# Optimization experiments

Measured on AMD Instinct MI355X. Metric: run time of the kernel, lower is better.

The kernel has to match this reference:

```python
import jax, jax.numpy as jnp
import numpy as np

PAD, BOS = 0, 1
EPS = 1e-08


def _lstm_cell(xt, h, c, wih, whh, bih, bhh):
    z = xt @ wih.T + h @ whh.T + bih + bhh
    i, f, g, o = jnp.split(z, 4, axis=-1)  # torch gate order i,f,g,o
    c = jax.nn.sigmoid(f) * c + jax.nn.sigmoid(i) * jnp.tanh(g)
    h = jax.nn.sigmoid(o) * jnp.tanh(c)
    return h, c


def _run_lstm(emb, wih, whh, bih, bhh):
    B, H = emb.shape[0], whh.shape[1]
    def step(carry, xt):
        h, c = _lstm_cell(xt, carry[0], carry[1], wih, whh, bih, bhh)
        return (h, c), h
    init = (jnp.zeros((B, H), emb.dtype), jnp.zeros((B, H), emb.dtype))
    (hT, cT), outs = jax.lax.scan(step, init, jnp.swapaxes(emb, 0, 1))
    return jnp.swapaxes(outs, 0, 1), hT, cT


def setup_inputs() -> dict:
    key = jax.random.key(0)
    V, H, B, S, T = 32000, 256, 8, 200, 51
    ks = jax.random.split(key, 24)
    def n(i, shape, s=0.02):
        return jax.random.normal(ks[i], shape, jnp.float32) * s
    x = jax.random.randint(ks[0], (B, S), 1, V)
    x = x.at[:, -1].set(V - 1)  # pins extended vocab size to 2V
    labels = jax.random.randint(ks[1], (B, T), 1, V)
    return {
        "x": x, "labels": labels, "ext_vocab_size": 2 * V,
        "emb_enc": n(2, (V, H)).at[PAD].set(0.0),
        "wih_f": n(3, (4 * H, H)), "whh_f": n(4, (4 * H, H)),
        "bih_f": jnp.zeros((4 * H,), jnp.float32), "bhh_f": jnp.zeros((4 * H,), jnp.float32),
        "wih_b": n(5, (4 * H, H)), "whh_b": n(6, (4 * H, H)),
        "bih_b": jnp.zeros((4 * H,), jnp.float32), "bhh_b": jnp.zeros((4 * H,), jnp.float32),
        "w_sel1": n(7, (H, 2 * H)), "b_sel1": jnp.zeros((H,), jnp.float32),
        "w_sel2": n(8, (1, H)), "b_sel2": jnp.zeros((1,), jnp.float32),
        "w_rh": n(9, (H, 2 * H)), "b_rh": jnp.zeros((H,), jnp.float32),
        "w_rc": n(10, (H, 2 * H)), "b_rc": jnp.zeros((H,), jnp.float32),
        "emb_dec": n(11, (V, H)).at[PAD].set(0.0),
        "wih_d": n(12, (4 * H, 3 * H)), "whh_d": n(13, (4 * H, H)),
        "bih_d": jnp.zeros((4 * H,), jnp.float32), "bhh_d": jnp.zeros((4 * H,), jnp.float32),
        "w_attn": n(14, (H, 4 * H)), "b_attn": jnp.zeros((H,), jnp.float32),
        "w_attn_v": n(15, (1, H)),
        "w_ptr": n(16, (1, 3 * H)), "b_ptr": jnp.zeros((1,), jnp.float32),
        "w_gen": n(17, (V, H)), "b_gen": jnp.zeros((V,), jnp.float32),
        "w_cov": n(18, (H, 1)), "b_cov": jnp.zeros((H,), jnp.float32),
    }


def reference(x, labels, ext_vocab_size, emb_enc, wih_f, whh_f, bih_f, bhh_f,
              wih_b, whh_b, bih_b, bhh_b, w_sel1, b_sel1, w_sel2, b_sel2,
              w_rh, b_rh, w_rc, b_rc, emb_dec, wih_d, whh_d, bih_d, bhh_d,
              w_attn, b_attn, w_attn_v, w_ptr, b_ptr, w_gen, b_gen, w_cov, b_cov):
    B, S = x.shape
    V, H = w_gen.shape
    # ---- Encoder: BiLSTM (no padding -> packing is identity; eval -> no dropout)
    emb = emb_enc[x]  # [B,S,H]
    out_f, h_f, c_f = _run_lstm(emb, wih_f, whh_f, bih_f, bhh_f)
    out_b_r, h_b, c_b = _run_lstm(emb[:, ::-1], wih_b, whh_b, bih_b, bhh_b)
    enc_out = jnp.concatenate([out_f, out_b_r[:, ::-1]], axis=-1)  # [B,S,2H]
    copy_probs = jax.nn.sigmoid(
        (jnp.tanh(enc_out @ w_sel1.T + b_sel1) @ w_sel2.T + b_sel2)[..., 0])  # [B,S]
    # ---- bidirectional state reduction
    h0 = jax.nn.relu(jnp.concatenate([h_f, h_b], -1) @ w_rh.T + b_rh)
    c0 = jax.nn.relu(jnp.concatenate([c_f, c_b], -1) @ w_rc.T + b_rc)
    # ---- Decoder loop (teacher forcing): inputs = [BOS, labels[:,1:T-1]]
    dec_in = jnp.concatenate(
        [jnp.full((B, 1), BOS, labels.dtype), labels[:, 1:-1]], axis=1)  # [B,T-1]
    mask_cp = (copy_probs > EPS).astype(jnp.float32)
    rows = jnp.arange(B)[:, None]

    def step(carry, tok):
        h, c, cov = carry
        cov_feat = cov[..., None] * w_cov[:, 0] + b_cov  # [B,S,H]
        feats = jnp.concatenate(
            [enc_out, jnp.broadcast_to(h[:, None, :], (B, S, H)), cov_feat], axis=-1)
        e = jnp.tanh(feats @ w_attn.T + b_attn)           # [B,S,H]
        attn = jax.nn.softmax(e @ w_attn_v[0], axis=1)    # [B,S]
        attn = attn * mask_cp
        attn = attn / (attn.sum(1, keepdims=True) + 1e-10)
        cov = cov + attn
        ctx = jnp.einsum('bs,bsd->bd', attn, enc_out)     # [B,2H]
        h, c = _lstm_cell(jnp.concatenate([emb_dec[tok], ctx], -1), h, c,
                          wih_d, whh_d, bih_d, bhh_d)
        p_gen = jax.nn.sigmoid(jnp.concatenate([ctx, h], -1) @ w_ptr.T + b_ptr)  # [B,1]
        vocab_dist = jax.nn.softmax(h @ w_gen.T + b_gen, axis=-1)  # [B,V]
        dist = jnp.zeros((B, ext_vocab_size), jnp.float32)
        dist = dist.at[:, :V].set(p_gen * vocab_dist)
        dist = dist.at[rows, x].add((1.0 - p_gen) * attn)  # pointer/copy scatter-add
        return (h, c, cov), dist

    cov0 = jnp.zeros((B, S), jnp.float32)
    _, outs = jax.lax.scan(step, (h0, c0, cov0), dec_in.T)
    outputs = jnp.swapaxes(outs, 0, 1)  # [B,T-1,EV]
    # ---- loss (faithful: CE treats the mixture distribution as logits)
    targets = labels[:, 1:]
    logp = jax.nn.log_softmax(outputs, axis=-1)
    nll = -jnp.take_along_axis(logp, targets[..., None], axis=-1)[..., 0]
    valid = (targets != PAD).astype(jnp.float32)
    loss_ce = (nll * valid).sum() / valid.sum()
    m = (x != PAD).astype(jnp.float32)
    lp = jnp.clip(jnp.log(copy_probs), -100.0, None)
    l1p = jnp.clip(jnp.log1p(-copy_probs), -100.0, None)
    bce = -(m * lp + (1.0 - m) * l1p)
    loss = loss_ce + 1.0 * (bce * m).sum() / m.sum()
    return outputs, loss
```

## Files before the change

### kernel.cpp

```cpp
#include <hip/hip_runtime.h>
#include <hip/hip_bf16.h>
#include <stdint.h>


#define DEVI __device__ __forceinline__
#define AT_RLX __ATOMIC_RELAXED
#define SC_AGT __HIP_MEMORY_SCOPE_AGENT

static constexpr size_t OFF_ACC   = 0;
static constexpr size_t OFF_FLAGE = 4;
static constexpr size_t OFF_FLAGD = 36;
static constexpr size_t ZERO_FLOATS = 200;
static constexpr size_t OFF_CTX   = 256;
static constexpr size_t OFF_EMB   = 4352;
static constexpr size_t OFF_HSEL  = OFF_EMB;
static constexpr size_t OFF_PREF  = OFF_EMB  + 409600;
static constexpr size_t OFF_PREB  = OFF_PREF + 1638400;
static constexpr size_t OFF_BIAS  = OFF_PREB + 1638400;
static constexpr size_t OFF_HB    = OFF_BIAS + 3072;
static constexpr size_t OFF_HFIN  = OFF_HB   + 8192;
static constexpr size_t OFF_CFIN  = OFF_HFIN + 4096;
static constexpr size_t OFF_ENCOUT= OFF_CFIN + 4096;
static constexpr size_t OFF_MASK  = OFF_ENCOUT + 819200;
static constexpr size_t OFF_C0    = OFF_MASK + 1600;
static constexpr size_t OFF_EP    = OFF_C0   + 2048;
static constexpr size_t OFF_WCP   = OFF_EP   + 409600;
static constexpr size_t OFF_BCP   = OFF_WCP  + 256;
static constexpr size_t OFF_DEMB  = OFF_BCP  + 256;
static constexpr size_t OFF_DPRE  = OFF_DEMB + 102400;
static constexpr size_t OFF_HBUF  = OFF_DPRE + 409600;
static constexpr size_t OFF_CS    = OFF_HBUF + 4096;
static constexpr size_t OFF_HS    = OFF_CS   + 204800;
static constexpr size_t OFF_AS    = OFF_HS   + 102400;
static constexpr size_t OFF_PG    = OFF_AS   + 80000;
static constexpr size_t OFF_PE    = OFF_PG   + 512;

DEVI float sigf(float x)      { return 1.0f / (1.0f + __expf(-x)); }
DEVI float tanh_fast(float x) { return 1.0f - 2.0f / (1.0f + __expf(2.0f * x)); }
DEVI float pick4(float z, float x1, float x2, float x3, int mm) {
  return mm == 0 ? z : (mm == 1 ? x1 : (mm == 2 ? x2 : x3));
}
DEVI float ald(const float* p)  { return __hip_atomic_load((float*)p, AT_RLX, SC_AGT); }
DEVI void  ast(float* p, float v){ __hip_atomic_store(p, v, AT_RLX, SC_AGT); }

DEVI void fbar(int* flags, int g, int n, int val) {
  __syncthreads();
  if ((int)threadIdx.x == 0)
    __hip_atomic_store(flags + g, val, AT_RLX, SC_AGT);
  if ((int)threadIdx.x < n && (int)threadIdx.x != g) {
    while (__hip_atomic_load(flags + threadIdx.x, AT_RLX, SC_AGT) < val)
      __builtin_amdgcn_s_sleep(1);
  }
  __syncthreads();
}

__global__ __launch_bounds__(256) void k_biassum(
    const float* bih_f, const float* bhh_f, const float* bih_b, const float* bhh_b,
    const float* bih_d, const float* bhh_d, float* ws) {
  int i = blockIdx.x * 256 + threadIdx.x;
  int which = i >> 10, jj = i & 1023;
  float v = (which == 0) ? bih_f[jj] + bhh_f[jj]
          : (which == 1) ? bih_b[jj] + bhh_b[jj]
                         : bih_d[jj] + bhh_d[jj];
  ws[OFF_BIAS + i] = v;
}

__global__ __launch_bounds__(256) void k_embed(
    const int* xin, const int* labels, const float* emb_enc, const float* emb_dec, float* ws) {
  int r = blockIdx.x, h = threadIdx.x;
  if (r < 1600) {
    int t = r >> 3, b = r & 7;
    ws[OFF_EMB + (size_t)r * 256 + h] = emb_enc[(size_t)xin[b * 200 + t] * 256 + h];
  } else {
    int r2 = r - 1600;
    int t = r2 >> 3, b = r2 & 7;
    int tok = (t == 0) ? 1 : labels[b * 51 + t];
    ws[OFF_DEMB + (size_t)r2 * 256 + h] = emb_dec[(size_t)tok * 256 + h];
  }
}

template<int BM, int BN, int TM, int TN, int CMAP, int ACT, int AMAP>
__global__ __launch_bounds__(256) void k_gemm(
    const float* __restrict__ A, const float* __restrict__ B,
    const float* __restrict__ bias, float* __restrict__ C,
    int M, int K, int ldb, int ldc) {
  __shared__ float As[16][BM];
  __shared__ float Bs[16][BN];
  const int tid = threadIdx.x;
  const int tx = tid & 15, ty = tid >> 4;
  const int m0 = blockIdx.x * BM, n0 = blockIdx.y * BN;
  float acc[TM][TN];
#pragma unroll
  for (int i = 0; i < TM; ++i)
#pragma unroll
    for (int q = 0; q < TN; ++q) acc[i][q] = 0.f;

  for (int kk = 0; kk < K; kk += 16) {
#pragma unroll
    for (int e = tid; e < BM * 4; e += 256) {
      int m = e >> 2, k4 = (e & 3) * 4;
      int gm0 = m0 + m;
      float4 v = {0.f, 0.f, 0.f, 0.f};
      if (gm0 < M) {
        int gm = AMAP ? (((199 - (gm0 >> 3)) << 3) + (gm0 & 7)) : gm0;
        v = *(const float4*)(A + (size_t)gm * K + kk + k4);
      }
      As[k4 + 0][m] = v.x; As[k4 + 1][m] = v.y; As[k4 + 2][m] = v.z; As[k4 + 3][m] = v.w;
    }
#pragma unroll
    for (int e = tid; e < BN * 4; e += 256) {
      int n = e >> 2, k4 = (e & 3) * 4;
      float4 v = *(const float4*)(B + (size_t)(n0 + n) * ldb + kk + k4);
      Bs[k4 + 0][n] = v.x; Bs[k4 + 1][n] = v.y; Bs[k4 + 2][n] = v.z; Bs[k4 + 3][n] = v.w;
    }
    __syncthreads();
#pragma unroll
    for (int k = 0; k < 16; ++k) {
      float a[TM], bv[TN];
#pragma unroll
      for (int i = 0; i < TM; ++i) a[i] = As[k][ty * TM + i];
#pragma unroll
      for (int q = 0; q < TN; ++q) bv[q] = Bs[k][tx * TN + q];
#pragma unroll
      for (int i = 0; i < TM; ++i)
#pragma unroll
        for (int q = 0; q < TN; ++q) acc[i][q] += a[i] * bv[q];
    }
    __syncthreads();
  }
#pragma unroll
  for (int i = 0; i < TM; ++i) {
    int gm = m0 + ty * TM + i;
    if (gm >= M) continue;
    size_t base;
    if (CMAP == 1) { int t = gm >> 3, b = gm & 7; base = (size_t)(b * 50 + t) * 64000; }
    else            base = (size_t)gm * ldc;
#pragma unroll
    for (int q = 0; q < TN; ++q) {
      int n = n0 + tx * TN + q;
      float v = acc[i][q] + bias[n];
      if (ACT == 1) v = tanh_fast(v);
      C[base + n] = v;
    }
  }
}

__global__ __launch_bounds__(512, 1) void k_encoder(
    const float* __restrict__ whh_f, const float* __restrict__ whh_b, float* __restrict__ ws) {
  __shared__ float hs[8 * 288];
  __shared__ float zs[512];
  const int dir = blockIdx.x >> 4;
  const int p   = blockIdx.x & 15;
  const int u0  = p * 16;
  const float* whh = dir ? whh_b : whh_f;
  const float* pre = ws + (dir ? OFF_PREB : OFF_PREF);
  int* flags = (int*)(ws + OFF_FLAGE) + dir * 16;
  const int tid = threadIdx.x;
  const int r = tid >> 3, kc = tid & 7;
  const int gt = r >> 4, ui = r & 15;
  const int j = gt * 256 + u0 + ui;
  float4 W[8];
  {
    const float* wr = whh + (size_t)j * 256 + kc * 32;
#pragma unroll
    for (int q = 0; q < 8; ++q) W[q] = *(const float4*)(wr + q * 4);
  }
  const int ui2 = tid & 15, b2 = tid >> 4;
  float c_reg = 0.f;
  float* hBa = ws + OFF_HB;
  float* enc = ws + OFF_ENCOUT;

  for (int t = 0; t < 200; ++t) {
    float pre_v = pre[((size_t)t * 8 + kc) * 1024 + j];
    float acc[8];
#pragma unroll
    for (int b = 0; b < 8; ++b) acc[b] = 0.f;
    if (t > 0) {
      {
        float* src = hBa + (size_t)((((t + 1) & 1) * 2 + dir) * 2048) + tid * 4;
        float v0 = ald(src + 0);
        float v1 = ald(src + 1);
        float v2 = ald(src + 2);
        float v3 = ald(src + 3);
        int kk0 = (tid * 4) & 255, bb = tid >> 6;
        float* dst = &hs[bb * 288 + (kk0 >> 5) * 36 + (kk0 & 31)];
        dst[0] = v0; dst[1] = v1; dst[2] = v2; dst[3] = v3;
      }
      __syncthreads();
      const float* hrow = &hs[kc * 36];
#pragma unroll
      for (int b = 0; b < 8; ++b) {
        const float* hbp = hrow + b * 288;
#pragma unroll
        for (int q = 0; q < 8; ++q) {
          float4 h4 = *(const float4*)(hbp + q * 4);
          acc[b] = fmaf(W[q].x, h4.x, acc[b]);
          acc[b] = fmaf(W[q].y, h4.y, acc[b]);
          acc[b] = fmaf(W[q].z, h4.z, acc[b]);
          acc[b] = fmaf(W[q].w, h4.w, acc[b]);
        }
      }
    }
    {
      bool h4b = (kc & 4) != 0;
#pragma unroll
      for (int i = 0; i < 4; ++i) {
        float send = h4b ? acc[i] : acc[i + 4];
        float keep = h4b ? acc[i + 4] : acc[i];
        acc[i] = keep + __shfl_xor(send, 4);
      }
      bool h2b = (kc & 2) != 0;
#pragma unroll
      for (int i = 0; i < 2; ++i) {
        float send = h2b ? acc[i] : acc[i + 2];
        float keep = h2b ? acc[i + 2] : acc[i];
        acc[i] = keep + __shfl_xor(send, 2);
      }
      bool h1b = (kc & 1) != 0;
      {
        float send = h1b ? acc[0] : acc[1];
        float keep = h1b ? acc[1] : acc[0];
        acc[0] = keep + __shfl_xor(send, 1);
      }
    }
    zs[tid] = acc[0] + pre_v;
    __syncthreads();
    if (tid < 128) {
      int i0 = ui2 * 8 + b2;
      float zi = zs[i0], zf = zs[128 + i0], zg = zs[256 + i0], zo = zs[384 + i0];
      float cn = sigf(zf) * c_reg + sigf(zi) * tanh_fast(zg);
      float hn = sigf(zo) * tanh_fast(cn);
      c_reg = cn;
      int uu = u0 + ui2;
      ast(hBa + (size_t)(((t & 1) * 2 + dir) * 2048) + b2 * 256 + uu, hn);
      int s = dir ? (199 - t) : t;
      enc[((size_t)b2 * 200 + s) * 512 + dir * 256 + uu] = hn;
      if (t == 199) {
        ws[OFF_HFIN + (size_t)(dir * 8 + b2) * 256 + uu] = hn;
        ws[OFF_CFIN + (size_t)(dir * 8 + b2) * 256 + uu] = cn;
      }
    }
    if (t < 199) fbar(flags, p, 16, t + 1);
  }
}

__global__ __launch_bounds__(64) void k_selbce(
    const float* w_sel2, const float* b_sel2, const int* xin, float* ws) {
  int r = blockIdx.x, lane = threadIdx.x;
  float pacc = 0.f;
#pragma unroll
  for (int i = 0; i < 4; ++i) {
    int k = lane + 64 * i;
    pacc += ws[OFF_HSEL + (size_t)r * 256 + k] * w_sel2[k];
  }
#pragma unroll
  for (int m = 1; m < 64; m <<= 1) pacc += __shfl_xor(pacc, m);
  if (lane == 0) {
    float cp = sigf(pacc + b_sel2[0]);
    ws[OFF_MASK + r] = (cp > 1e-8f) ? 1.f : 0.f;
    int b = r / 200, s = r % 200;
    float m = (xin[b * 200 + s] != 0) ? 1.f : 0.f;
    if (m > 0.f) {
      float lp = fmaxf(logf(cp), -100.f);
      atomicAdd(ws + OFF_ACC + 2, -lp);
    }
    atomicAdd(ws + OFF_ACC + 3, m);
  }
}

__global__ __launch_bounds__(256) void k_wcp(
    const float* w_attn, const float* w_cov, const float* b_cov, float* ws) {
  int jj = threadIdx.x;
  float a = 0.f, c = 0.f;
  for (int h = 0; h < 256; ++h) {
    float w = w_attn[(size_t)jj * 1024 + 768 + h];
    a += w * w_cov[h];
    c += w * b_cov[h];
  }
  ws[OFF_WCP + jj] = a;
  ws[OFF_BCP + jj] = c;
}

__global__ __launch_bounds__(256) void k_h0c0(
    const float* w_rh, const float* b_rh, const float* w_rc, const float* b_rc, float* ws) {
  int b = blockIdx.x, jj = threadIdx.x;
  const float* hf  = ws + OFF_HFIN + (size_t)b * 256;
  const float* hbk = ws + OFF_HFIN + 2048 + (size_t)b * 256;
  const float* cf  = ws + OFF_CFIN + (size_t)b * 256;
  const float* cbk = ws + OFF_CFIN + 2048 + (size_t)b * 256;
  float ah = b_rh[jj], ac = b_rc[jj];
  for (int k = 0; k < 256; ++k) {
    ah += hf[k] * w_rh[(size_t)jj * 512 + k];
    ac += cf[k] * w_rc[(size_t)jj * 512 + k];
  }
  for (int k = 0; k < 256; ++k) {
    ah += hbk[k] * w_rh[(size_t)jj * 512 + 256 + k];
    ac += cbk[k] * w_rc[(size_t)jj * 512 + 256 + k];
  }
  ws[OFF_C0 + (size_t)b * 256 + jj] = fmaxf(ac, 0.f);
  ws[OFF_HBUF + (size_t)b * 256 + jj] = fmaxf(ah, 0.f);
}

__global__ __launch_bounds__(512, 1) void k_decoder(
    const float* __restrict__ wih_d, const float* __restrict__ whh_d,
    const float* __restrict__ w_attn, const float* __restrict__ w_attn_v,
    float* __restrict__ ws) {
  __shared__ float hc_s[8 * 768];
  __shared__ float h_pad[264];
  __shared__ float hw_q[64];
  __shared__ float e_s[256];
  __shared__ float at_s[256], cv_s[256], msk_s[256];
  __shared__ float zs_l[256];
  __shared__ float wcq_s[64], bcq_s[64], wvq_s[64];
  __shared__ float mS_s[2];
  const int g = blockIdx.x, tid = threadIdx.x;
  const int b1 = g >> 2, sq = g & 3, s0 = sq * 50;
  int* flags = (int*)(ws + OFF_FLAGD);
  const int jl = tid >> 3, kq = tid & 7;
  const int kseg = tid & 15, row_l = tid >> 4;
  const int u_l = row_l & 7, gate = row_l >> 3;
  const int j = gate * 256 + g * 8 + u_l;
  float4 W48[12];
#pragma unroll
  for (int q = 0; q < 12; ++q) {
    int k0 = 4 * kseg + 64 * q;
    W48[q] = (k0 < 512) ? *(const float4*)(wih_d + (size_t)j * 768 + 256 + k0)
                        : *(const float4*)(whh_d + (size_t)j * 256 + (k0 - 512));
  }
  float4 W32[8];
  {
    const float* wsrc = w_attn + (size_t)(sq * 64 + jl) * 1024 + 512 + kq * 32;
#pragma unroll
    for (int q = 0; q < 8; ++q) W32[q] = *(const float4*)(wsrc + q * 4);
  }
  const int u_c = tid & 7, b_c = tid >> 3;
  float c_reg = (tid < 64) ? ws[OFF_C0 + (size_t)b_c * 256 + g * 8 + u_c] : 0.f;
  for (int s = tid; s < 256; s += 512) {
    msk_s[s] = (s < 200) ? ws[OFF_MASK + b1 * 200 + s] : 0.f;
    cv_s[s] = 0.f;
  }
  if (tid < 64) {
    wcq_s[tid] = ws[OFF_WCP + sq * 64 + tid];
    bcq_s[tid] = ws[OFF_BCP + sq * 64 + tid];
    wvq_s[tid] = w_attn_v[sq * 64 + tid];
  }
  __syncthreads();

  for (int t = 0; t < 50; ++t) {
    const int rb = t & 1, wb = 1 - rb;
    if (tid < 128) ast(ws + OFF_CTX + g * 128 + tid, 0.f);
    if (tid < 256) {
      float v = ald(ws + OFF_HBUF + (size_t)rb * 2048 + b1 * 256 + tid);
      h_pad[(tid >> 5) * 33 + (tid & 31)] = v;
    }
    __syncthreads();
    {
      float a = 0.f;
      const float* hp = &h_pad[kq * 33 * 4 / 4];
      const float* hq = &h_pad[kq * 33];
#pragma unroll
      for (int q = 0; q < 8; ++q) {
        float4 h4 = { hq[q * 4 + 0], hq[q * 4 + 1], hq[q * 4 + 2], hq[q * 4 + 3] };
        a = fmaf(W32[q].x, h4.x, a);
        a = fmaf(W32[q].y, h4.y, a);
        a = fmaf(W32[q].z, h4.z, a);
        a = fmaf(W32[q].w, h4.w, a);
      }
      (void)hp;
      a += __shfl_xor(a, 1);
      a += __shfl_xor(a, 2);
      a += __shfl_xor(a, 4);
      if (kq == 0) hw_q[jl] = a;
    }
    __syncthreads();
    if (tid < 200) {
      const int s = tid;
      float cv = cv_s[s];
      const float* ep = ws + OFF_EP + ((size_t)(b1 * 200 + s)) * 256 + sq * 64;
      float pe = 0.f;
#pragma unroll
      for (int i4 = 0; i4 < 16; ++i4) {
        float4 e4 = *(const float4*)(ep + i4 * 4);
        float4 h4 = *(const float4*)(&hw_q[i4 * 4]);
        float4 w4 = *(const float4*)(&wcq_s[i4 * 4]);
        float4 b4 = *(const float4*)(&bcq_s[i4 * 4]);
        float4 v4 = *(const float4*)(&wvq_s[i4 * 4]);
        pe = fmaf(tanh_fast(e4.x + h4.x + cv * w4.x + b4.x), v4.x, pe);
        pe = fmaf(tanh_fast(e4.y + h4.y + cv * w4.y + b4.y), v4.y, pe);
        pe = fmaf(tanh_fast(e4.z + h4.z + cv * w4.z + b4.z), v4.z, pe);
        pe = fmaf(tanh_fast(e4.w + h4.w + cv * w4.w + b4.w), v4.w, pe);
      }
      ast(ws + OFF_PE + (size_t)(sq * 8 + b1) * 200 + s, pe);
    }
    fbar(flags, g, 32, 3 * t + 1);

    if (tid < 200) {
      float e0 = ald(ws + OFF_PE + (size_t)(0 * 8 + b1) * 200 + tid);
      float e1 = ald(ws + OFF_PE + (size_t)(1 * 8 + b1) * 200 + tid);
      float e2 = ald(ws + OFF_PE + (size_t)(2 * 8 + b1) * 200 + tid);
      float e3 = ald(ws + OFF_PE + (size_t)(3 * 8 + b1) * 200 + tid);
      e_s[tid] = (e0 + e1) + (e2 + e3);
    }
    __syncthreads();
    if (tid < 64) {
      float m = -1e30f;
#pragma unroll
      for (int i = 0; i < 4; ++i) {
        int s = tid + 64 * i;
        if (s < 200) m = fmaxf(m, e_s[s]);
      }
#pragma unroll
      for (int md = 1; md < 64; md <<= 1) m = fmaxf(m, __shfl_xor(m, md));
      float es = 0.f, ems = 0.f;
#pragma unroll
      for (int i = 0; i < 4; ++i) {
        int s = tid + 64 * i;
        if (s < 200) {
          float e = __expf(e_s[s] - m);
          es += e; ems += e * msk_s[s];
        }
      }
#pragma unroll
      for (int md = 1; md < 64; md <<= 1) { es += __shfl_xor(es, md); ems += __shfl_xor(ems, md); }
      if (tid == 0) { mS_s[0] = m; mS_s[1] = 1.0f / (ems + 1e-10f * es); }
    }
    __syncthreads();
    if (tid < 200) {
      float a = __expf(e_s[tid] - mS_s[0]) * msk_s[tid] * mS_s[1];
      at_s[tid] = a;
      cv_s[tid] += a;
      if (tid >= s0 && tid < s0 + 50)
        ws[OFF_AS + ((size_t)t * 8 + b1) * 200 + tid] = a;
    }
    __syncthreads();
    {
      float ca = 0.f;
      const float* ebase = ws + OFF_ENCOUT + ((size_t)(b1 * 200 + s0)) * 512 + tid;
#pragma unroll 10
      for (int s2 = 0; s2 < 50; ++s2)
        ca = fmaf(at_s[s0 + s2], ebase[(size_t)s2 * 512], ca);
      atomicAdd(ws + OFF_CTX + b1 * 512 + tid, ca);
    }
    fbar(flags, g, 32, 3 * t + 2);

    for (int e = tid; e < 6144; e += 512) {
      int bb = e / 768, kk2 = e % 768;
      hc_s[e] = (kk2 < 512) ? ald(ws + OFF_CTX + bb * 512 + kk2)
                            : ald(ws + OFF_HBUF + (size_t)rb * 2048 + bb * 256 + (kk2 - 512));
    }
    __syncthreads();
    if (g < 8) ws[OFF_CS + ((size_t)t * 8 + g) * 512 + tid] = hc_s[g * 768 + tid];
    float acc[8];
#pragma unroll
    for (int b = 0; b < 8; ++b) acc[b] = 0.f;
#pragma unroll
    for (int q = 0; q < 12; ++q) {
      int k0 = 4 * kseg + 64 * q;
#pragma unroll
      for (int b = 0; b < 8; ++b) {
        float4 h4 = *(const float4*)(&hc_s[b * 768 + k0]);
        acc[b] = fmaf(W48[q].x, h4.x, acc[b]);
        acc[b] = fmaf(W48[q].y, h4.y, acc[b]);
        acc[b] = fmaf(W48[q].z, h4.z, acc[b]);
        acc[b] = fmaf(W48[q].w, h4.w, acc[b]);
      }
    }
    {
      bool h8 = (kseg & 8) != 0;
#pragma unroll
      for (int i = 0; i < 4; ++i) {
        float send = h8 ? acc[i] : acc[i + 4];
        float keep = h8 ? acc[i + 4] : acc[i];
        acc[i] = keep + __shfl_xor(send, 8);
      }
      bool h4b = (kseg & 4) != 0;
#pragma unroll
      for (int i = 0; i < 2; ++i) {
        float send = h4b ? acc[i] : acc[i + 2];
        float keep = h4b ? acc[i + 2] : acc[i];
        acc[i] = keep + __shfl_xor(send, 4);
      }
      bool h2b = (kseg & 2) != 0;
      {
        float send = h2b ? acc[0] : acc[1];
        float keep = h2b ? acc[1] : acc[0];
        acc[0] = keep + __shfl_xor(send, 2);
      }
      acc[0] += __shfl_xor(acc[0], 1);
    }
    {
      int bz = kseg >> 1;
      float z = acc[0] + ws[OFF_DPRE + ((size_t)t * 8 + bz) * 1024 + j];
      if ((kseg & 1) == 0) zs_l[row_l * 8 + bz] = z;
    }
    __syncthreads();
    if (tid < 64) {
      float zi = zs_l[(0  + u_c) * 8 + b_c];
      float zf = zs_l[(8  + u_c) * 8 + b_c];
      float zg = zs_l[(16 + u_c) * 8 + b_c];
      float zo = zs_l[(24 + u_c) * 8 + b_c];
      float cn = sigf(zf) * c_reg + sigf(zi) * tanh_fast(zg);
      float hn = sigf(zo) * tanh_fast(cn);
      c_reg = cn;
      ast(ws + OFF_HBUF + (size_t)wb * 2048 + b_c * 256 + g * 8 + u_c, hn);
      ws[OFF_HS + ((size_t)t * 8 + b_c) * 256 + g * 8 + u_c] = hn;
    }
    fbar(flags, g, 32, 3 * t + 3);
  }
}

__global__ __launch_bounds__(64) void k_pgen(const float* w_ptr, const float* b_ptr, float* ws) {
  int r = blockIdx.x, lane = threadIdx.x;
  float p = 0.f;
#pragma unroll
  for (int i = 0; i < 12; ++i) {
    int k = lane + 64 * i;
    float v = (k < 512) ? ws[OFF_CS + (size_t)r * 512 + k]
                        : ws[OFF_HS + (size_t)r * 256 + (k - 512)];
    p += v * w_ptr[k];
  }
#pragma unroll
  for (int m = 1; m < 64; m <<= 1) p += __shfl_xor(p, m);
  if (lane == 0) ws[OFF_PG + r] = sigf(p + b_ptr[0]);
}

__global__ __launch_bounds__(256) void k_v2(const int* xin, const int* labels, float* ws, float* out) {
  __shared__ float redm[256], reds[256];
  __shared__ int xv[200];
  __shared__ float s1sh, corrsh;
  int r = blockIdx.x, tid = threadIdx.x;
  int tt = r >> 3, b = r & 7;
  float* row = out + (size_t)(b * 50 + tt) * 64000;
  for (int i = tid; i < 200; i += 256) xv[i] = xin[b * 200 + i];
  float m = -1e30f, s = 0.f;
  for (int i = tid; i < 32000; i += 256) {
    float z = row[i];
    float nm = fmaxf(m, z);
    s = s * __expf(m - nm) + __expf(z - nm);
    m = nm;
  }
  redm[tid] = m; reds[tid] = s;
  __syncthreads();
  for (int st = 128; st >= 1; st >>= 1) {
    if (tid < st) {
      float m2 = redm[tid + st], s2 = reds[tid + st];
      float M = fmaxf(redm[tid], m2);
      reds[tid] = reds[tid] * __expf(redm[tid] - M) + s2 * __expf(m2 - M);
      redm[tid] = M;
    }
    __syncthreads();
  }
  float mx = redm[0], sum = reds[0];
  float pg = ws[OFF_PG + r];
  __syncthreads();
  float s1 = 0.f;
  float inv = 1.0f / sum;
  for (int i = tid; i < 32000; i += 256) {
    float z = row[i];
    float d = pg * (__expf(z - mx) * inv);
    row[i] = d;
    s1 += __expf(d);
  }
  for (int i = 32000 + tid; i < 64000; i += 256) row[i] = 0.0f;
  reds[tid] = s1;
  __syncthreads();
  for (int st = 128; st >= 1; st >>= 1) { if (tid < st) reds[tid] += reds[tid + st]; __syncthreads(); }
  if (tid == 0) { s1sh = reds[0]; corrsh = 0.f; }
  __syncthreads();
  if (tid < 200) {
    int v = xv[tid];
    bool own = true;
    for (int s2 = 0; s2 < tid; ++s2) if (xv[s2] == v) { own = false; break; }
    if (own) {
      float delta = 0.f;
      for (int s2 = tid; s2 < 200; ++s2)
        if (xv[s2] == v) delta += ws[OFF_AS + (size_t)r * 200 + s2];
      delta *= (1.0f - pg);
      float base = row[v];
      row[v] = base + delta;
      atomicAdd(&corrsh, __expf(base + delta) - __expf(base));
    }
  }
  __syncthreads();
  if (tid == 0) {
    float lse = logf(s1sh + corrsh + 32000.0f);
    int tgt = labels[b * 51 + tt + 1];
    float dt = row[tgt];
    float valid = (tgt != 0) ? 1.f : 0.f;
    atomicAdd(ws + OFF_ACC + 0, valid * (lse - dt));
    atomicAdd(ws + OFF_ACC + 1, valid);
  }
}

__global__ void k_loss(float* ws, float* out, int out_size) {
  out[out_size - 1] = ws[OFF_ACC + 0] / ws[OFF_ACC + 1] + ws[OFF_ACC + 2] / ws[OFF_ACC + 3];
}

extern "C" void kernel_launch(void* const* d_in, const int* in_sizes, int n_in,
                              void* d_out, int out_size, void* d_ws, size_t ws_size,
                              hipStream_t stream) {
  (void)in_sizes; (void)n_in; (void)ws_size;
  const int*   x       = (const int*)  d_in[0];
  const int*   labels  = (const int*)  d_in[1];
  const float* emb_enc = (const float*)d_in[3];
  const float* wih_f   = (const float*)d_in[4];
  const float* whh_f   = (const float*)d_in[5];
  const float* bih_f   = (const float*)d_in[6];
  const float* bhh_f   = (const float*)d_in[7];
  const float* wih_b   = (const float*)d_in[8];
  const float* whh_b   = (const float*)d_in[9];
  const float* bih_b   = (const float*)d_in[10];
  const float* bhh_b   = (const float*)d_in[11];
  const float* w_sel1  = (const float*)d_in[12];
  const float* b_sel1  = (const float*)d_in[13];
  const float* w_sel2  = (const float*)d_in[14];
  const float* b_sel2  = (const float*)d_in[15];
  const float* w_rh    = (const float*)d_in[16];
  const float* b_rh    = (const float*)d_in[17];
  const float* w_rc    = (const float*)d_in[18];
  const float* b_rc    = (const float*)d_in[19];
  const float* emb_dec = (const float*)d_in[20];
  const float* wih_d   = (const float*)d_in[21];
  const float* whh_d   = (const float*)d_in[22];
  const float* bih_d   = (const float*)d_in[23];
  const float* bhh_d   = (const float*)d_in[24];
  const float* w_attn  = (const float*)d_in[25];
  const float* b_attn  = (const float*)d_in[26];
  const float* w_attn_v= (const float*)d_in[27];
  const float* w_ptr   = (const float*)d_in[28];
  const float* b_ptr   = (const float*)d_in[29];
  const float* w_gen   = (const float*)d_in[30];
  const float* b_gen   = (const float*)d_in[31];
  const float* w_cov   = (const float*)d_in[32];
  const float* b_cov   = (const float*)d_in[33];
  float* ws  = (float*)d_ws;
  float* out = (float*)d_out;

  hipMemsetAsync(d_ws, 0, ZERO_FLOATS * 4, stream);
  k_biassum<<<12, 256, 0, stream>>>(bih_f, bhh_f, bih_b, bhh_b, bih_d, bhh_d, ws);
  k_embed<<<2000, 256, 0, stream>>>(x, labels, emb_enc, emb_dec, ws);
  k_gemm<64,64,4,4,0,0,0><<<dim3(25,16), 256, 0, stream>>>(ws+OFF_EMB,  wih_f, ws+OFF_BIAS,      ws+OFF_PREF, 1600, 256, 256, 1024);
  k_gemm<64,64,4,4,0,0,1><<<dim3(25,16), 256, 0, stream>>>(ws+OFF_EMB,  wih_b, ws+OFF_BIAS+1024, ws+OFF_PREB, 1600, 256, 256, 1024);
  k_gemm<64,64,4,4,0,0,0><<<dim3(7,16),  256, 0, stream>>>(ws+OFF_DEMB, wih_d, ws+OFF_BIAS+2048, ws+OFF_DPRE, 400,  256, 768, 1024);
  k_encoder<<<32, 512, 0, stream>>>(whh_f, whh_b, ws);
  k_gemm<64,64,4,4,0,1,0><<<dim3(25,4),  256, 0, stream>>>(ws+OFF_ENCOUT, w_sel1, b_sel1, ws+OFF_HSEL, 1600, 512, 512, 256);
  k_selbce<<<1600, 64, 0, stream>>>(w_sel2, b_sel2, x, ws);
  k_gemm<64,64,4,4,0,0,0><<<dim3(25,4),  256, 0, stream>>>(ws+OFF_ENCOUT, w_attn, b_attn, ws+OFF_EP, 1600, 512, 1024, 256);
  k_wcp<<<1, 256, 0, stream>>>(w_attn, w_cov, b_cov, ws);
  k_h0c0<<<8, 256, 0, stream>>>(w_rh, b_rh, w_rc, b_rc, ws);
  k_decoder<<<32, 512, 0, stream>>>(wih_d, whh_d, w_attn, w_attn_v, ws);
  k_pgen<<<400, 64, 0, stream>>>(w_ptr, b_ptr, ws);
  k_gemm<128,128,8,8,1,0,0><<<dim3(4,250), 256, 0, stream>>>(ws+OFF_HS, w_gen, b_gen, out, 400, 256, 256, 64000);
  k_v2<<<400, 256, 0, stream>>>(x, labels, ws, out);
  k_loss<<<1, 1, 0, stream>>>(ws, out, out_size);
}
```

Baseline: 2.356 ms.

## Replace encoder flag barrier with epoch-tagged hidden-state values

After: 2.314 ms. About the same (-1.8%).

```diff
diff --git a/kernel.cpp b/kernel.cpp
--- a/kernel.cpp
+++ b/kernel.cpp
@@ -14,6 +14,7 @@
 static constexpr size_t OFF_CTX   = 256;
 static constexpr size_t OFF_EMB   = 4352;
 static constexpr size_t OFF_HSEL  = OFF_EMB;
+static constexpr size_t OFF_HP    = OFF_EMB;
 static constexpr size_t OFF_PREF  = OFF_EMB  + 409600;
 static constexpr size_t OFF_PREB  = OFF_PREF + 1638400;
 static constexpr size_t OFF_BIAS  = OFF_PREB + 1638400;
@@ -37,9 +38,6 @@
 
 DEVI float sigf(float x)      { return 1.0f / (1.0f + __expf(-x)); }
 DEVI float tanh_fast(float x) { return 1.0f - 2.0f / (1.0f + __expf(2.0f * x)); }
-DEVI float pick4(float z, float x1, float x2, float x3, int mm) {
-  return mm == 0 ? z : (mm == 1 ? x1 : (mm == 2 ? x2 : x3));
-}
 DEVI float ald(const float* p)  { return __hip_atomic_load((float*)p, AT_RLX, SC_AGT); }
 DEVI void  ast(float* p, float v){ __hip_atomic_store(p, v, AT_RLX, SC_AGT); }
 
@@ -154,7 +152,7 @@
   const int u0  = p * 16;
   const float* whh = dir ? whh_b : whh_f;
   const float* pre = ws + (dir ? OFF_PREB : OFF_PREF);
-  int* flags = (int*)(ws + OFF_FLAGE) + dir * 16;
+  unsigned long long* hp = (unsigned long long*)(ws + OFF_HP);
   const int tid = threadIdx.x;
   const int r = tid >> 3, kc = tid & 7;
   const int gt = r >> 4, ui = r & 15;
@@ -167,7 +165,6 @@
   }
   const int ui2 = tid & 15, b2 = tid >> 4;
   float c_reg = 0.f;
-  float* hBa = ws + OFF_HB;
   float* enc = ws + OFF_ENCOUT;
 
   for (int t = 0; t < 200; ++t) {
@@ -177,14 +174,24 @@
     for (int b = 0; b < 8; ++b) acc[b] = 0.f;
     if (t > 0) {
       {
-        float* src = hBa + (size_t)((((t + 1) & 1) * 2 + dir) * 2048) + tid * 4;
-        float v0 = ald(src + 0);
-        float v1 = ald(src + 1);
-        float v2 = ald(src + 2);
-        float v3 = ald(src + 3);
+        unsigned long long* src = hp + (size_t)((((t + 1) & 1) * 2 + dir) * 2048) + tid * 4;
+        const unsigned long long e = (unsigned long long)(unsigned)t;
+        unsigned long long a0, a1, a2, a3;
+        for (;;) {
+          a0 = __hip_atomic_load(src + 0, AT_RLX, SC_AGT);
+          a1 = __hip_atomic_load(src + 1, AT_RLX, SC_AGT);
+          a2 = __hip_atomic_load(src + 2, AT_RLX, SC_AGT);
+          a3 = __hip_atomic_load(src + 3, AT_RLX, SC_AGT);
+          if (((a0 >> 32) == e) && ((a1 >> 32) == e) &&
+              ((a2 >> 32) == e) && ((a3 >> 32) == e)) break;
+          __builtin_amdgcn_s_sleep(1);
+        }
         int kk0 = (tid * 4) & 255, bb = tid >> 6;
         float* dst = &hs[bb * 288 + (kk0 >> 5) * 36 + (kk0 & 31)];
-        dst[0] = v0; dst[1] = v1; dst[2] = v2; dst[3] = v3;
+        dst[0] = __uint_as_float((unsigned)a0);
+        dst[1] = __uint_as_float((unsigned)a1);
+        dst[2] = __uint_as_float((unsigned)a2);
+        dst[3] = __uint_as_float((unsigned)a3);
       }
       __syncthreads();
       const float* hrow = &hs[kc * 36];
@@ -232,7 +239,13 @@
       float hn = sigf(zo) * tanh_fast(cn);
       c_reg = cn;
       int uu = u0 + ui2;
-      ast(hBa + (size_t)(((t & 1) * 2 + dir) * 2048) + b2 * 256 + uu, hn);
+      if (t < 199) {
+        unsigned long long pk =
+            ((unsigned long long)(unsigned)(t + 1) << 32) |
+            (unsigned long long)__float_as_uint(hn);
+        __hip_atomic_store(hp + (size_t)(((t & 1) * 2 + dir) * 2048) + b2 * 256 + uu,
+                           pk, AT_RLX, SC_AGT);
+      }
       int s = dir ? (199 - t) : t;
       enc[((size_t)b2 * 200 + s) * 512 + dir * 256 + uu] = hn;
       if (t == 199) {
@@ -240,7 +253,6 @@
         ws[OFF_CFIN + (size_t)(dir * 8 + b2) * 256 + uu] = cn;
       }
     }
-    if (t < 199) fbar(flags, p, 16, t + 1);
   }
 }
 
@@ -356,7 +368,6 @@
     __syncthreads();
     {
       float a = 0.f;
-      const float* hp = &h_pad[kq * 33 * 4 / 4];
       const float* hq = &h_pad[kq * 33];
 #pragma unroll
       for (int q = 0; q < 8; ++q) {
@@ -366,7 +377,6 @@
         a = fmaf(W32[q].z, h4.z, a);
         a = fmaf(W32[q].w, h4.w, a);
       }
-      (void)hp;
       a += __shfl_xor(a, 1);
       a += __shfl_xor(a, 2);
       a += __shfl_xor(a, 4);
@@ -642,6 +652,7 @@
   k_gemm<64,64,4,4,0,0,0><<<dim3(25,16), 256, 0, stream>>>(ws+OFF_EMB,  wih_f, ws+OFF_BIAS,      ws+OFF_PREF, 1600, 256, 256, 1024);
   k_gemm<64,64,4,4,0,0,1><<<dim3(25,16), 256, 0, stream>>>(ws+OFF_EMB,  wih_b, ws+OFF_BIAS+1024, ws+OFF_PREB, 1600, 256, 256, 1024);
   k_gemm<64,64,4,4,0,0,0><<<dim3(7,16),  256, 0, stream>>>(ws+OFF_DEMB, wih_d, ws+OFF_BIAS+2048, ws+OFF_DPRE, 400,  256, 768, 1024);
+  hipMemsetAsync((void*)(ws + OFF_HP), 0, (size_t)2 * 2 * 2048 * sizeof(unsigned long long), stream);
   k_encoder<<<32, 512, 0, stream>>>(whh_f, whh_b, ws);
   k_gemm<64,64,4,4,0,1,0><<<dim3(25,4),  256, 0, stream>>>(ws+OFF_ENCOUT, w_sel1, b_sel1, ws+OFF_HSEL, 1600, 512, 512, 256);
   k_selbce<<<1600, 64, 0, stream>>>(w_sel2, b_sel2, x, ws);
```
